# Performance work log

Measured on AMD Instinct MI355X. Metric: run time of the kernel, lower is better.

Reference implementation:

```python
import math
import jax, jax.numpy as jnp
import numpy as np

D_MODEL, N_HEADS, QKV, D_HEAD, D_FF, N_BLOCKS, IN_DIM = 288, 8, 328, 41, 1315, 4, 83
B, S = 1024, 128
EPS = 1e-5


def setup_inputs() -> dict:
    key = jax.random.key(0)
    ks = iter(jax.random.split(key, 64))
    def rn(shape, scale=0.05):
        return jax.random.normal(next(ks), shape, jnp.float32) * scale
    inp = {
        "x": jax.random.normal(next(ks), (B, S, IN_DIM), jnp.float32),
        "Wp": rn((D_MODEL, IN_DIM)), "bp": rn((D_MODEL,)),
        "phase": rn((D_MODEL,)),
        "Wq": rn((N_BLOCKS, QKV, D_MODEL)), "bq": rn((N_BLOCKS, QKV)),
        "Wk": rn((N_BLOCKS, QKV, D_MODEL)), "bk": rn((N_BLOCKS, QKV)),
        "Wv": rn((N_BLOCKS, QKV, D_MODEL)), "bv": rn((N_BLOCKS, QKV)),
        "Wo": rn((N_BLOCKS, D_MODEL, QKV)), "bo": rn((N_BLOCKS, D_MODEL)),
        "temp": jnp.ones((N_BLOCKS,), jnp.float32) + rn((N_BLOCKS,), 0.01),
        "qscale": jnp.ones((N_BLOCKS, N_HEADS), jnp.float32) + rn((N_BLOCKS, N_HEADS), 0.01),
        "Wf1": rn((N_BLOCKS, D_FF, D_MODEL)), "bf1": rn((N_BLOCKS, D_FF)),
        "Wf2": rn((N_BLOCKS, D_MODEL, D_FF)), "bf2": rn((N_BLOCKS, D_MODEL)),
        "n1w": jnp.ones((N_BLOCKS, D_MODEL), jnp.float32), "n1b": jnp.zeros((N_BLOCKS, D_MODEL), jnp.float32),
        "n2w": jnp.ones((N_BLOCKS, D_MODEL), jnp.float32), "n2b": jnp.zeros((N_BLOCKS, D_MODEL), jnp.float32),
        "skip": jnp.ones((N_BLOCKS,), jnp.float32),
        "bn_w": jnp.ones((D_MODEL,), jnp.float32), "bn_b": jnp.zeros((D_MODEL,), jnp.float32),
        "bn_mean": rn((D_MODEL,)), "bn_var": jax.random.uniform(next(ks), (D_MODEL,), jnp.float32, 0.5, 1.5),
        "h1w": rn((144, D_MODEL)), "h1b": rn((144,)),
        "h2w": rn((72, 144)), "h2b": rn((72,)),
        "h3w": rn((1, 72)), "h3b": rn((1,)),
        "u1w": rn((72, D_MODEL)), "u1b": rn((72,)),
        "u2w": rn((1, 72)), "u2b": rn((1,)),
    }
    return inp


def _layer_norm(x, w, b):
    mu = jnp.mean(x, axis=-1, keepdims=True)
    var = jnp.mean((x - mu) ** 2, axis=-1, keepdims=True)
    return (x - mu) * jax.lax.rsqrt(var + EPS) * w + b


def reference(x, Wp, bp, phase, Wq, bq, Wk, bk, Wv, bv, Wo, bo, temp, qscale,
              Wf1, bf1, Wf2, bf2, n1w, n1b, n2w, n2b, skip,
              bn_w, bn_b, bn_mean, bn_var,
              h1w, h1b, h2w, h2b, h3w, h3b, u1w, u1b, u2w, u2b):
    Bsz, Sl, _ = x.shape
    # input projection
    h = jnp.einsum('bsi,di->bsd', x, Wp) + bp
    # sinusoidal positional encoding modulated by cos(quantum_phase)
    pos = jnp.arange(Sl, dtype=jnp.float32)[:, None]
    div = jnp.exp(jnp.arange(0, D_MODEL, 2, dtype=jnp.float32) * (-math.log(10000.0) / D_MODEL))
    pe = jnp.zeros((Sl, D_MODEL), jnp.float32)
    pe = pe.at[:, 0::2].set(jnp.sin(pos * div)).at[:, 1::2].set(jnp.cos(pos * div))
    h = h + pe * jnp.cos(phase)

    for l in range(N_BLOCKS):
        # attention with temperature-scaled softmax + post-softmax per-head scale
        q = (jnp.einsum('bsd,qd->bsq', h, Wq[l]) + bq[l]).reshape(Bsz, Sl, N_HEADS, D_HEAD)
        k = (jnp.einsum('bsd,qd->bsq', h, Wk[l]) + bk[l]).reshape(Bsz, Sl, N_HEADS, D_HEAD)
        v = (jnp.einsum('bsd,qd->bsq', h, Wv[l]) + bv[l]).reshape(Bsz, Sl, N_HEADS, D_HEAD)
        scale = math.sqrt(D_HEAD) * temp[l]
        scores = jnp.einsum('bqhd,bkhd->bhqk', q, k) / scale  # [B,H,S,S]
        attn = jax.nn.softmax(scores, axis=-1) * qscale[l][None, :, None, None]
        o = jnp.einsum('bhqk,bkhd->bqhd', attn, v).reshape(Bsz, Sl, QKV)
        o = jnp.einsum('bsq,dq->bsd', o, Wo[l]) + bo[l]
        h = _layer_norm(h + skip[l] * o, n1w[l], n1b[l])
        # GELU FFN (exact erf gelu, dropout inactive in eval)
        f = jax.nn.gelu(jnp.einsum('bsd,fd->bsf', h, Wf1[l]) + bf1[l], approximate=False)
        f = jnp.einsum('bsf,df->bsd', f, Wf2[l]) + bf2[l]
        h = _layer_norm(h + f, n2w[l], n2b[l])

    pooled = jnp.mean(h, axis=1)  # [B, D_MODEL]
    # output head: BatchNorm1d (eval, running stats) -> GELU -> MLP
    z = (pooled - bn_mean) * jax.lax.rsqrt(bn_var + EPS) * bn_w + bn_b
    z = jax.nn.gelu(z, approximate=False)
    z = jax.nn.gelu(z @ h1w.T + h1b, approximate=False)
    z = jax.nn.gelu(z @ h2w.T + h2b, approximate=False)
    pred = z @ h3w.T + h3b  # [B, 1]
    # uncertainty head
    u = jax.nn.relu(pooled @ u1w.T + u1b)
    unc = jax.nn.softplus(u @ u2w.T + u2b)  # [B, 1]
    return pred, unc
```

## Files before the change

kernel.cpp:

```cpp
#include <hip/hip_runtime.h>
#include <cstdint>

typedef __attribute__((ext_vector_type(8))) short short8;
typedef __attribute__((ext_vector_type(4))) short s4v;
typedef __attribute__((ext_vector_type(4))) float floatx4;

#define DEV __device__ __forceinline__

DEV short f2bf(float f) {
  unsigned u = __builtin_bit_cast(unsigned, f);
  u += 0x7fffu + ((u >> 16) & 1u);
  return (short)(u >> 16);
}
DEV short f2bf_ru(float f) {
  unsigned u = __builtin_bit_cast(unsigned, f);
  return (short)((u + 0x8000u) >> 16);
}
DEV float bf2f(short s) {
  unsigned u = ((unsigned)(unsigned short)s) << 16;
  return __builtin_bit_cast(float, u);
}
DEV float gelu_exact(float x) {
  return 0.5f * x * (1.0f + erff(x * 0.70710678118654752f));
}
DEV float gelu_fast(float x) {
  const float t2 = 1.5957691216057308f * (x + 0.044715f * x * x * x);
  return x / (1.0f + __expf(-t2));
}
DEV void gload16(const void* g, void* l) {
  __builtin_amdgcn_global_load_lds((const __attribute__((address_space(1))) void*)g,
                                   (__attribute__((address_space(3))) void*)l,
                                   16, 0, 0);
}

DEV int stage_col64(int row, int g) {
  return ((g >> 2) ^ (row & 1)) * 32 + (((g & 3) ^ ((row >> 1) & 3))) * 8;
}
DEV int frag_off64(int R, int s, int quad) {
  return R * 64 + ((((s ^ (R & 1)) << 2) | (quad ^ ((R >> 1) & 3)))) * 8;
}

template<int MODE>
__global__ __launch_bounds__(256)
void gemm_kernel(const short* __restrict__ A, const short* __restrict__ Bw,
                 const float* __restrict__ bias, short* __restrict__ C,
                 const float* __restrict__ pe,
                 int K, int lda, int ldb, int ldc, int Nstore, int NT, long hstride)
{
  __shared__ __align__(16) short lds[128 * 136];
  short* Ct = lds;

  const int tid  = threadIdx.x;
  const int wave = tid >> 6, lane = tid & 63;
  const int quad = lane >> 4, r16 = lane & 15;
  const int per = gridDim.x >> 3;
  const int gti = (blockIdx.x & 7) * per + (blockIdx.x >> 3);
  const int mt = gti / NT, nt = gti - mt * NT;
  const int wm = (wave >> 1) * 64, wn = (wave & 1) * 64;

  const long Abase = (long)mt * 128 * lda;
  const long Bbase = (long)nt * 128 * ldb;

  floatx4 acc[4][4] = {};

  int k0 = 0;
  for (; k0 + 64 <= K; k0 += 64) {
    __syncthreads();
#pragma unroll
    for (int j = 0; j < 8; ++j) {
      const int c2 = tid + j * 256;
      const int cb = c2 & 1023;
      const int row = cb >> 3, g = cb & 7;
      const int col = stage_col64(row, g);
      const short* src = (c2 < 1024) ? (A  + Abase + (long)row * lda + k0 + col)
                                     : (Bw + Bbase + (long)row * ldb + k0 + col);
      gload16(src, &lds[(size_t)(c2 & ~63) * 8]);
    }
    __syncthreads();

#pragma unroll
    for (int s = 0; s < 2; ++s) {
      short8 af[4], bfr[4];
#pragma unroll
      for (int i = 0; i < 4; ++i) {
        const int R = wm + i * 16 + r16;
        af[i] = *(const short8*)&lds[frag_off64(R, s, quad)];
      }
#pragma unroll
      for (int j = 0; j < 4; ++j) {
        const int R = wn + j * 16 + r16;
        bfr[j] = *(const short8*)&lds[8192 + frag_off64(R, s, quad)];
      }
#pragma unroll
      for (int i = 0; i < 4; ++i)
#pragma unroll
        for (int j = 0; j < 4; ++j)
          acc[i][j] = __builtin_amdgcn_mfma_f32_16x16x32_bf16(bfr[j], af[i], acc[i][j], 0, 0, 0);
    }
  }

  if (k0 < K) {
    short* As = lds;
    short* Bs = lds + 128 * 32;
    const int row0 = tid >> 2,         cc0 = (tid & 3) ^ ((row0 >> 1) & 3);
    const int row1 = (256 + tid) >> 2, cc1 = ((256 + tid) & 3) ^ ((row1 >> 1) & 3);
    __syncthreads();
    gload16(A  + Abase + (long)row0 * lda + k0 + cc0 * 8, &As[(0 * 256 + wave * 64) * 8]);
    gload16(A  + Abase + (long)row1 * lda + k0 + cc1 * 8, &As[(1 * 256 + wave * 64) * 8]);
    gload16(Bw + Bbase + (long)row0 * ldb + k0 + cc0 * 8, &Bs[(0 * 256 + wave * 64) * 8]);
    gload16(Bw + Bbase + (long)row1 * ldb + k0 + cc1 * 8, &Bs[(1 * 256 + wave * 64) * 8]);
    __syncthreads();

    short8 af[4], bfr[4];
#pragma unroll
    for (int i = 0; i < 4; ++i) {
      const int R = wm + i * 16 + r16;
      af[i] = *(const short8*)&As[R * 32 + (quad ^ ((R >> 1) & 3)) * 8];
    }
#pragma unroll
    for (int j = 0; j < 4; ++j) {
      const int R = wn + j * 16 + r16;
      bfr[j] = *(const short8*)&Bs[R * 32 + (quad ^ ((R >> 1) & 3)) * 8];
    }
#pragma unroll
    for (int i = 0; i < 4; ++i)
#pragma unroll
      for (int j = 0; j < 4; ++j)
        acc[i][j] = __builtin_amdgcn_mfma_f32_16x16x32_bf16(bfr[j], af[i], acc[i][j], 0, 0, 0);
  }

  const int mb0 = mt * 128, tb = nt * 128;

  __syncthreads();
#pragma unroll
  for (int j = 0; j < 4; ++j) {
    const int n0 = wn + j * 16 + quad * 4;
    const floatx4 b4 = *(const floatx4*)&bias[tb + n0];
#pragma unroll
    for (int i = 0; i < 4; ++i) {
      const int m = wm + i * 16 + r16;
      floatx4 v = acc[i][j] + b4;
      if (MODE == 1) {
#pragma unroll
        for (int rg = 0; rg < 4; ++rg) v[rg] = gelu_fast(v[rg]);
      }
      if (MODE == 2) {
        const floatx4 p4 = *(const floatx4*)&pe[((mb0 + m) & 127) * 384 + tb + n0];
        v = v + p4;
      }
      s4v o4;
#pragma unroll
      for (int rg = 0; rg < 4; ++rg) o4[rg] = f2bf_ru(v[rg]);
      *(s4v*)&Ct[m * 136 + n0] = o4;
    }
  }
  __syncthreads();

#pragma unroll
  for (int rr = 0; rr < 8; ++rr) {
    const int chunk = rr * 256 + tid;
    const int row = chunk >> 4, ch = chunk & 15;
    const int gcol = tb + ch * 8;
    if (MODE == 3) {
      const int g = gcol / 48, d0 = gcol - g * 48;
      *(short8*)(C + (long)g * hstride + (long)(mb0 + row) * 48 + d0) =
          *(const short8*)&Ct[row * 136 + ch * 8];
    } else if (gcol < Nstore) {
      *(short8*)(C + (long)(mb0 + row) * ldc + gcol) = *(const short8*)&Ct[row * 136 + ch * 8];
    }
  }
}

template<bool AHEAD>
__global__ __launch_bounds__(512, 4)
void gemm_ln_kernel(const short* __restrict__ A, const short* __restrict__ Bw,
                    const float* __restrict__ bias, short* __restrict__ h,
                    const float* __restrict__ lnw, const float* __restrict__ lnb,
                    const float* __restrict__ skip_p, int layer, int use_skip,
                    int K, int lda, int ldb, long ahs)
{
  __shared__ __align__(16) short lds[128 * 296];
  __shared__ float redp[4][2][2][16];
  __shared__ float reds[4][2][2][16];
  short* Hs = lds;

  const int tid  = threadIdx.x;
  const int wave = tid >> 6, lane = tid & 63;
  const int quad = lane >> 4, r16 = lane & 15;
  const int wr = wave >> 1, wc = wave & 1;
  const int mt = blockIdx.x;
  const long mrow0 = (long)mt * 128;

  floatx4 acc[2][9] = {};

  auto stage = [&](short* buf, int k0) {
    for (int c = tid; c < 1664; c += 512) {
      const void* src;
      if (c < 512) {
        const int row = c >> 2, cc = (c & 3) ^ ((row >> 1) & 3);
        if (AHEAD) {
          const int kc = k0 + cc * 8;
          const int g = kc / 48, d = kc - g * 48;
          src = A + (long)g * ahs + (mrow0 + row) * 48 + d;
        } else {
          src = A + (mrow0 + row) * lda + k0 + cc * 8;
        }
      } else {
        const int cb = c - 512;
        const int row = cb >> 2, cc = (cb & 3) ^ ((row >> 1) & 3);
        src = Bw + (long)row * ldb + k0 + cc * 8;
      }
      gload16(src, &buf[(size_t)(c & ~63) * 8]);
    }
  };

  auto compute = [&](const short* buf) {
    const short* As_ = buf;
    const short* Bs_ = buf + 4096;
    const int Ra0 = wr * 32 + r16, Ra1 = Ra0 + 16;
    const short8 af0 = *(const short8*)&As_[Ra0 * 32 + (quad ^ ((Ra0 >> 1) & 3)) * 8];
    const short8 af1 = *(const short8*)&As_[Ra1 * 32 + (quad ^ ((Ra1 >> 1) & 3)) * 8];
#pragma unroll
    for (int t = 0; t < 9; ++t) {
      const int Rb = wc * 144 + t * 16 + r16;
      const short8 b = *(const short8*)&Bs_[Rb * 32 + (quad ^ ((Rb >> 1) & 3)) * 8];
      acc[0][t] = __builtin_amdgcn_mfma_f32_16x16x32_bf16(b, af0, acc[0][t], 0, 0, 0);
      acc[1][t] = __builtin_amdgcn_mfma_f32_16x16x32_bf16(b, af1, acc[1][t], 0, 0, 0);
    }
  };

  short* const B0 = lds;
  short* const B1 = lds + 13312;

  stage(B0, 0);
  __syncthreads();
  int k0 = 0;
  while (true) {
    if (k0 + 32 < K) stage(B1, k0 + 32);
    compute(B0);
    __syncthreads();
    k0 += 32;
    if (k0 >= K) break;
    if (k0 + 32 < K) stage(B0, k0 + 32);
    compute(B1);
    __syncthreads();
    k0 += 32;
    if (k0 >= K) break;
  }

  for (int c = tid; c < 4608; c += 512) {
    const int row = c / 36, ch = c - row * 36;
    *(short8*)&Hs[row * 296 + ch * 8] =
        *(const short8*)(h + (mrow0 + row) * 288 + ch * 8);
  }
  __syncthreads();

  const float skipv = use_skip ? skip_p[layer] : 1.0f;
  const int m0 = wr * 32 + r16, m1 = m0 + 16;

  float ps0 = 0.f, ss0 = 0.f, ps1 = 0.f, ss1 = 0.f;
#pragma unroll
  for (int t = 0; t < 9; ++t) {
    const int n0 = wc * 144 + t * 16 + quad * 4;
    const floatx4 b4 = *(const floatx4*)&bias[n0];
    const s4v h40 = *(const s4v*)&Hs[m0 * 296 + n0];
    const s4v h41 = *(const s4v*)&Hs[m1 * 296 + n0];
#pragma unroll
    for (int rg = 0; rg < 4; ++rg) {
      const float y0 = bf2f(h40[rg]) + skipv * (acc[0][t][rg] + b4[rg]);
      const float y1 = bf2f(h41[rg]) + skipv * (acc[1][t][rg] + b4[rg]);
      acc[0][t][rg] = y0; acc[1][t][rg] = y1;
      ps0 += y0; ss0 += y0 * y0;
      ps1 += y1; ss1 += y1 * y1;
    }
  }
  ps0 += __shfl_xor(ps0, 16); ps0 += __shfl_xor(ps0, 32);
  ss0 += __shfl_xor(ss0, 16); ss0 += __shfl_xor(ss0, 32);
  ps1 += __shfl_xor(ps1, 16); ps1 += __shfl_xor(ps1, 32);
  ss1 += __shfl_xor(ss1, 16); ss1 += __shfl_xor(ss1, 32);
  if (lane < 16) {
    redp[wr][wc][0][r16] = ps0; redp[wr][wc][1][r16] = ps1;
    reds[wr][wc][0][r16] = ss0; reds[wr][wc][1][r16] = ss1;
  }
  __syncthreads();
  const float psum0 = redp[wr][0][0][r16] + redp[wr][1][0][r16];
  const float psum1 = redp[wr][0][1][r16] + redp[wr][1][1][r16];
  const float ssum0 = reds[wr][0][0][r16] + reds[wr][1][0][r16];
  const float ssum1 = reds[wr][0][1][r16] + reds[wr][1][1][r16];
  const float mean0 = psum0 * (1.f / 288.f), mean1 = psum1 * (1.f / 288.f);
  const float rstd0 = rsqrtf(ssum0 * (1.f / 288.f) - mean0 * mean0 + 1e-5f);
  const float rstd1 = rsqrtf(ssum1 * (1.f / 288.f) - mean1 * mean1 + 1e-5f);

#pragma unroll
  for (int t = 0; t < 9; ++t) {
    const int n0 = wc * 144 + t * 16 + quad * 4;
    const floatx4 w4 = *(const floatx4*)&lnw[n0];
    const floatx4 l4 = *(const floatx4*)&lnb[n0];
    s4v o0, o1;
#pragma unroll
    for (int rg = 0; rg < 4; ++rg) {
      o0[rg] = f2bf_ru((acc[0][t][rg] - mean0) * rstd0 * w4[rg] + l4[rg]);
      o1[rg] = f2bf_ru((acc[1][t][rg] - mean1) * rstd1 * w4[rg] + l4[rg]);
    }
    *(s4v*)&Hs[m0 * 296 + n0] = o0;
    *(s4v*)&Hs[m1 * 296 + n0] = o1;
  }
  __syncthreads();

  for (int c = tid; c < 4608; c += 512) {
    const int row = c / 36, ch = c - row * 36;
    *(short8*)(h + (mrow0 + row) * 288 + ch * 8) =
        *(const short8*)&Hs[row * 296 + ch * 8];
  }
}

__global__ __launch_bounds__(512, 2)
void ffn_kernel(short* __restrict__ h,
                const short* __restrict__ W1, const float* __restrict__ b1,
                const short* __restrict__ W2, const float* __restrict__ b2,
                const float* __restrict__ lnw, const float* __restrict__ lnb)
{
  __shared__ __align__(16) short lds[53248];
  __shared__ float redp[4][2][2][16];
  __shared__ float reds[4][2][2][16];
  short* const fl = lds + 36864;

  const int tid  = threadIdx.x;
  const int wave = tid >> 6, lane = tid & 63;
  const int quad = lane >> 4, r16 = lane & 15;
  const int wr = wave >> 1, wp = wave & 1;
  const long mrow0 = (long)blockIdx.x * 128;

  short8 ha[2][9];
#pragma unroll
  for (int i = 0; i < 2; ++i) {
    const long rb = (mrow0 + wr * 32 + i * 16 + r16) * 288L;
#pragma unroll
    for (int k9 = 0; k9 < 9; ++k9)
      ha[i][k9] = *(const short8*)(h + rb + k9 * 32 + quad * 8);
  }

  floatx4 acc2[2][9] = {};

  auto stageW1_64 = [&](int c, int kp, short* dst) {
#pragma unroll
    for (int j = 0; j < 2; ++j) {
      const int c2 = tid + j * 512;
      const int row = c2 >> 3, g = c2 & 7;
      gload16(W1 + ((long)(c * 128 + row)) * 288 + kp * 64 + stage_col64(row, g),
              &dst[(size_t)(c2 & ~63) * 8]);
    }
  };
  auto stageW1_32 = [&](int c, int k9, short* dst) {
    const int row = tid >> 2, cc = (tid & 3) ^ ((row >> 1) & 3);
    gload16(W1 + ((long)(c * 128 + row)) * 288 + k9 * 32 + cc * 8,
            &dst[(size_t)(tid & ~63) * 8]);
  };
  auto stageW2_64 = [&](int c, int kh, short* dst) {
#pragma unroll
    for (int j = 0; j < 5; ++j) {
      const int c2 = tid + j * 512;
      if (c2 < 2304) {
        const int row = c2 >> 3, g = c2 & 7;
        gload16(W2 + (long)row * 1408 + c * 128 + kh * 64 + stage_col64(row, g),
                &dst[(size_t)(c2 & ~63) * 8]);
      }
    }
  };

  short* const ring0 = lds;
  short* const ring1 = lds + 18432;

  stageW1_64(0, 0, ring0);
  __syncthreads();
  int cur = 0;

  for (int c = 0; c < 11; ++c) {
    floatx4 acc1[2][4] = {};

#pragma unroll
    for (int kp = 0; kp < 4; ++kp) {
      short* const Sn = cur ? ring0 : ring1;
      const short* Sc = cur ? ring1 : ring0;
      if (kp < 3) stageW1_64(c, kp + 1, Sn);
      else        stageW1_32(c, 8, Sn);

#pragma unroll
      for (int s = 0; s < 2; ++s) {
        short8 bfr[4];
#pragma unroll
        for (int j = 0; j < 4; ++j) {
          const int R = wp * 64 + j * 16 + r16;
          bfr[j] = *(const short8*)&Sc[frag_off64(R, s, quad)];
        }
#pragma unroll
        for (int i = 0; i < 2; ++i)
#pragma unroll
          for (int j = 0; j < 4; ++j)
            acc1[i][j] = __builtin_amdgcn_mfma_f32_16x16x32_bf16(bfr[j], ha[i][kp * 2 + s], acc1[i][j], 0, 0, 0);
      }
      __syncthreads();
      cur ^= 1;
    }

    {
      short* const Sn = cur ? ring0 : ring1;
      const short* Sc = cur ? ring1 : ring0;
      stageW2_64(c, 0, Sn);

      short8 bfr[4];
#pragma unroll
      for (int j = 0; j < 4; ++j) {
        const int R = wp * 64 + j * 16 + r16;
        bfr[j] = *(const short8*)&Sc[R * 32 + (quad ^ ((R >> 1) & 3)) * 8];
      }
#pragma unroll
      for (int i = 0; i < 2; ++i)
#pragma unroll
        for (int j = 0; j < 4; ++j)
          acc1[i][j] = __builtin_amdgcn_mfma_f32_16x16x32_bf16(bfr[j], ha[i][8], acc1[i][j], 0, 0, 0);

#pragma unroll
      for (int i = 0; i < 2; ++i) {
        const int m = wr * 32 + i * 16 + r16;
#pragma unroll
        for (int j = 0; j < 4; ++j) {
          const int nb = c * 128 + wp * 64 + j * 16 + quad * 4;
          const floatx4 b4 = *(const floatx4*)&b1[nb];
          s4v o;
#pragma unroll
          for (int rg = 0; rg < 4; ++rg)
            o[rg] = f2bf_ru(gelu_fast(acc1[i][j][rg] + b4[rg]));
          const int ks = wp * 2 + (j >> 1);
          const int mg = ((j & 1) * 2 + (quad >> 1)) ^ ((m >> 1) & 3);
          *(s4v*)&fl[ks * 4096 + m * 32 + mg * 8 + (quad & 1) * 4] = o;
        }
      }
      __syncthreads();
      cur ^= 1;
    }

#pragma unroll
    for (int sg = 0; sg < 2; ++sg) {
      short* const Sn = cur ? ring0 : ring1;
      const short* Sc = cur ? ring1 : ring0;
      if (sg == 0)     stageW2_64(c, 1, Sn);
      else if (c < 10) stageW1_64(c + 1, 0, Sn);

#pragma unroll
      for (int s = 0; s < 2; ++s) {
        const int ks = sg * 2 + s;
        short8 af2[2];
#pragma unroll
        for (int i = 0; i < 2; ++i) {
          const int R = wr * 32 + i * 16 + r16;
          af2[i] = *(const short8*)&fl[ks * 4096 + R * 32 + (quad ^ ((R >> 1) & 3)) * 8];
        }
        short8 br[9];
#pragma unroll
        for (int t = 0; t < 9; ++t) {
          const int R = wp * 144 + t * 16 + r16;
          br[t] = *(const short8*)&Sc[frag_off64(R, s, quad)];
        }
#pragma unroll
        for (int i = 0; i < 2; ++i)
#pragma unroll
          for (int t = 0; t < 9; ++t)
            acc2[i][t] = __builtin_amdgcn_mfma_f32_16x16x32_bf16(br[t], af2[i], acc2[i][t], 0, 0, 0);
      }
      __syncthreads();
      cur ^= 1;
    }
  }

  for (int c2 = tid; c2 < 4608; c2 += 512) {
    const int row = c2 / 36, ch = c2 - row * 36;
    *(short8*)&lds[row * 296 + ch * 8] =
        *(const short8*)(h + (mrow0 + row) * 288 + ch * 8);
  }
  __syncthreads();

  const int m0 = wr * 32 + r16, m1 = m0 + 16;
  float ps0 = 0.f, ss0 = 0.f, ps1 = 0.f, ss1 = 0.f;
#pragma unroll
  for (int t = 0; t < 9; ++t) {
    const int n0 = wp * 144 + t * 16 + quad * 4;
    const floatx4 b4 = *(const floatx4*)&b2[n0];
    const s4v h40 = *(const s4v*)&lds[m0 * 296 + n0];
    const s4v h41 = *(const s4v*)&lds[m1 * 296 + n0];
#pragma unroll
    for (int rg = 0; rg < 4; ++rg) {
      const float y0 = bf2f(h40[rg]) + acc2[0][t][rg] + b4[rg];
      const float y1 = bf2f(h41[rg]) + acc2[1][t][rg] + b4[rg];
      acc2[0][t][rg] = y0; acc2[1][t][rg] = y1;
      ps0 += y0; ss0 += y0 * y0;
      ps1 += y1; ss1 += y1 * y1;
    }
  }
  ps0 += __shfl_xor(ps0, 16); ps0 += __shfl_xor(ps0, 32);
  ss0 += __shfl_xor(ss0, 16); ss0 += __shfl_xor(ss0, 32);
  ps1 += __shfl_xor(ps1, 16); ps1 += __shfl_xor(ps1, 32);
  ss1 += __shfl_xor(ss1, 16); ss1 += __shfl_xor(ss1, 32);
  if (lane < 16) {
    redp[wr][wp][0][r16] = ps0; redp[wr][wp][1][r16] = ps1;
    reds[wr][wp][0][r16] = ss0; reds[wr][wp][1][r16] = ss1;
  }
  __syncthreads();
  const float psum0 = redp[wr][0][0][r16] + redp[wr][1][0][r16];
  const float psum1 = redp[wr][0][1][r16] + redp[wr][1][1][r16];
  const float ssum0 = reds[wr][0][0][r16] + reds[wr][1][0][r16];
  const float ssum1 = reds[wr][0][1][r16] + reds[wr][1][1][r16];
  const float mean0 = psum0 * (1.f / 288.f), mean1 = psum1 * (1.f / 288.f);
  const float rstd0 = rsqrtf(ssum0 * (1.f / 288.f) - mean0 * mean0 + 1e-5f);
  const float rstd1 = rsqrtf(ssum1 * (1.f / 288.f) - mean1 * mean1 + 1e-5f);

#pragma unroll
  for (int t = 0; t < 9; ++t) {
    const int n0 = wp * 144 + t * 16 + quad * 4;
    const floatx4 w4 = *(const floatx4*)&lnw[n0];
    const floatx4 l4 = *(const floatx4*)&lnb[n0];
    s4v o0, o1;
#pragma unroll
    for (int rg = 0; rg < 4; ++rg) {
      o0[rg] = f2bf_ru((acc2[0][t][rg] - mean0) * rstd0 * w4[rg] + l4[rg]);
      o1[rg] = f2bf_ru((acc2[1][t][rg] - mean1) * rstd1 * w4[rg] + l4[rg]);
    }
    *(s4v*)&lds[m0 * 296 + n0] = o0;
    *(s4v*)&lds[m1 * 296 + n0] = o1;
  }
  __syncthreads();

  for (int c2 = tid; c2 < 4608; c2 += 512) {
    const int row = c2 / 36, ch = c2 - row * 36;
    *(short8*)(h + (mrow0 + row) * 288 + ch * 8) =
        *(const short8*)&lds[row * 296 + ch * 8];
  }
}

__global__ __launch_bounds__(256)
void attn_kernel(short* __restrict__ qkv,
                 const float* __restrict__ qscale, int layer, long Mc)
{
  __shared__ __align__(16) short qk[2 * 128 * 72];
  __shared__ __align__(16) short vsT[48 * 136 + 32];
  __shared__ float red[2][2][64];

  short* qs = qk;
  short* ks = qk + 128 * 72;
  short* Pb = qk;

  const int b = blockIdx.x, h = blockIdx.y;
  const int tid = threadIdx.x;
  const long sec = Mc * 48;
  const short* qg = qkv + (long)h * sec + (long)b * 128 * 48;
  const short* kg = qg + 8 * sec;
  const short* vg = qg + 16 * sec;
  short* og = qkv + (long)(16 + h) * sec + (long)b * 128 * 48;

  for (int c = tid; c < 768; c += 256) {
    const int s = c / 6, dc = c - (c / 6) * 6;
    *(short8*)&qs[s * 72 + dc * 8] = *(const short8*)(qg + (long)s * 48 + dc * 8);
    *(short8*)&ks[s * 72 + dc * 8] = *(const short8*)(kg + (long)s * 48 + dc * 8);
  }
  {
    short8 z;
#pragma unroll
    for (int j = 0; j < 8; ++j) z[j] = 0;
    for (int c = tid; c < 384; c += 256) {
      const int s = c / 3, t = c - (c / 3) * 3;
      *(short8*)&qs[s * 72 + 48 + t * 8] = z;
      *(short8*)&ks[s * 72 + 48 + t * 8] = z;
    }
  }
  for (int c = tid; c < 768; c += 256) {
    const int s = c & 127, dc = c >> 7;
    const short8 tv = *(const short8*)(vg + (long)s * 48 + dc * 8);
#pragma unroll
    for (int j = 0; j < 8; ++j) {
      const int row = dc * 8 + j;
      vsT[row * 136 + ((row >> 3) & 3) * 8 + s] = tv[j];
    }
  }
  __syncthreads();

  const int wave = tid >> 6, lane = tid & 63;
  const int quad = lane >> 4, r16 = lane & 15;
  const int wm = (wave >> 1) * 64, wn = (wave & 1) * 64;
  const int rh = wave >> 1, ch = wave & 1;
  const float qsc = qscale[layer * 8 + h];

  floatx4 acc[4][4] = {};
#pragma unroll
  for (int kk = 0; kk < 2; ++kk) {
    const int k0 = kk * 32;
    short8 af[4], bfr[4];
#pragma unroll
    for (int i = 0; i < 4; ++i)
      af[i] = *(const short8*)&qs[(wm + i * 16 + r16) * 72 + k0 + quad * 8];
#pragma unroll
    for (int j = 0; j < 4; ++j)
      bfr[j] = *(const short8*)&ks[(wn + j * 16 + r16) * 72 + k0 + quad * 8];
#pragma unroll
    for (int i = 0; i < 4; ++i)
#pragma unroll
      for (int j = 0; j < 4; ++j)
        acc[i][j] = __builtin_amdgcn_mfma_f32_16x16x32_bf16(bfr[j], af[i], acc[i][j], 0, 0, 0);
  }

  float rmax[4], rsum[4];
#pragma unroll
  for (int i = 0; i < 4; ++i) {
    float m = acc[i][0][0];
#pragma unroll
    for (int j = 0; j < 4; ++j)
#pragma unroll
      for (int rg = 0; rg < 4; ++rg) m = fmaxf(m, acc[i][j][rg]);
    m = fmaxf(m, __shfl_xor(m, 16));
    m = fmaxf(m, __shfl_xor(m, 32));
    rmax[i] = m;
  }
  if (lane < 16)
#pragma unroll
    for (int i = 0; i < 4; ++i) red[rh][ch][i * 16 + r16] = rmax[i];
  __syncthreads();
#pragma unroll
  for (int i = 0; i < 4; ++i)
    rmax[i] = fmaxf(red[rh][0][i * 16 + r16], red[rh][1][i * 16 + r16]);

#pragma unroll
  for (int i = 0; i < 4; ++i) {
    float s = 0.f;
#pragma unroll
    for (int j = 0; j < 4; ++j)
#pragma unroll
      for (int rg = 0; rg < 4; ++rg) {
        const float e = __expf(acc[i][j][rg] - rmax[i]);
        acc[i][j][rg] = e;
        s += e;
      }
    s += __shfl_xor(s, 16);
    s += __shfl_xor(s, 32);
    rsum[i] = s;
  }
  __syncthreads();
  if (lane < 16)
#pragma unroll
    for (int i = 0; i < 4; ++i) red[rh][ch][i * 16 + r16] = rsum[i];
  __syncthreads();
#pragma unroll
  for (int i = 0; i < 4; ++i)
    rmax[i] = qsc / (red[rh][0][i * 16 + r16] + red[rh][1][i * 16 + r16]);

#pragma unroll
  for (int i = 0; i < 4; ++i) {
    const int sq = wm + i * 16 + r16;
#pragma unroll
    for (int j = 0; j < 4; ++j) {
      const int sk0 = wn + j * 16 + quad * 4;
      s4v p4;
#pragma unroll
      for (int rg = 0; rg < 4; ++rg) p4[rg] = f2bf_ru(acc[i][j][rg] * rmax[i]);
      *(s4v*)&Pb[sq * 136 + sk0] = p4;
    }
  }
  __syncthreads();

  const int om = (wave >> 1) * 64, on = (wave & 1) * 32;
  const int jn = (on == 0) ? 2 : 1;
  floatx4 oacc[4][2] = {};
  for (int kk = 0; kk < 4; ++kk) {
    const int k0 = kk * 32;
    short8 af[4], bfr[2];
#pragma unroll
    for (int i = 0; i < 4; ++i)
      af[i] = *(const short8*)&Pb[(om + i * 16 + r16) * 136 + k0 + quad * 8];
    for (int j = 0; j < jn; ++j) {
      const int row = on + j * 16 + r16;
      bfr[j] = *(const short8*)&vsT[row * 136 + ((row >> 3) & 3) * 8 + k0 + quad * 8];
    }
#pragma unroll
    for (int i = 0; i < 4; ++i)
      for (int j = 0; j < jn; ++j)
        oacc[i][j] = __builtin_amdgcn_mfma_f32_16x16x32_bf16(bfr[j], af[i], oacc[i][j], 0, 0, 0);
  }
#pragma unroll
  for (int i = 0; i < 4; ++i)
    for (int j = 0; j < jn; ++j) {
      const int d0 = on + j * 16 + quad * 4;
      const int sq = om + i * 16 + r16;
      s4v o4;
#pragma unroll
      for (int rg = 0; rg < 4; ++rg) o4[rg] = f2bf_ru(oacc[i][j][rg]);
      *(s4v*)(og + (long)sq * 48 + d0) = o4;
    }
}

__global__ __launch_bounds__(256)
void head_kernel(const short* __restrict__ hb, float* __restrict__ out,
                 const float* bn_w, const float* bn_b, const float* bn_mean, const float* bn_var,
                 const float* h1w, const float* h1b, const float* h2w, const float* h2b,
                 const float* h3w, const float* h3b,
                 const float* u1w, const float* u1b, const float* u2w, const float* u2b)
{
  __shared__ float psum[252][8];
  __shared__ float pooled[288], z[288], z1[144], z2[72], uu[72];
  const int b = blockIdx.x, tid = threadIdx.x;

  if (tid < 252) {
    const int cch = tid % 36, grp = tid / 36;
    float a[8];
#pragma unroll
    for (int j = 0; j < 8; ++j) a[j] = 0.f;
    for (int r = grp; r < 128; r += 7) {
      const short8 hv = *(const short8*)(hb + ((long)b * 128 + r) * 288 + cch * 8);
#pragma unroll
      for (int j = 0; j < 8; ++j) a[j] += bf2f(hv[j]);
    }
#pragma unroll
    for (int j = 0; j < 8; ++j) psum[tid][j] = a[j];
  }
  __syncthreads();
  for (int d = tid; d < 288; d += 256) {
    const int cch = d >> 3, j = d & 7;
    float s = 0.f;
#pragma unroll
    for (int g = 0; g < 7; ++g) s += psum[g * 36 + cch][j];
    pooled[d] = s * (1.f / 128.f);
  }
  __syncthreads();

  for (int d = tid; d < 288; d += 256) {
    const float p = pooled[d];
    z[d] = gelu_exact((p - bn_mean[d]) * rsqrtf(bn_var[d] + 1e-5f) * bn_w[d] + bn_b[d]);
  }
  __syncthreads();

  if (tid < 144) {
    float s = h1b[tid];
    for (int k = 0; k < 288; ++k) s += z[k] * h1w[tid * 288 + k];
    z1[tid] = gelu_exact(s);
  } else if (tid < 216) {
    const int t = tid - 144;
    float s = u1b[t];
    for (int k = 0; k < 288; ++k) s += pooled[k] * u1w[t * 288 + k];
    uu[t] = fmaxf(s, 0.f);
  }
  __syncthreads();

  if (tid < 72) {
    float s = h2b[tid];
    for (int k = 0; k < 144; ++k) s += z1[k] * h2w[tid * 144 + k];
    z2[tid] = gelu_exact(s);
  }
  __syncthreads();

  if (tid == 0) {
    float s = h3b[0];
    for (int k = 0; k < 72; ++k) s += z2[k] * h3w[k];
    out[b] = s;
  }
  if (tid == 64) {
    float s = u2b[0];
    for (int k = 0; k < 72; ++k) s += uu[k] * u2w[k];
    out[1024 + b] = (s > 20.f) ? s : log1pf(__expf(s));
  }
}

__global__ void conv_w_kernel(const float* __restrict__ src, short* __restrict__ dst,
                              int N, int K, int Npad, int Kpad, int total)
{
  const int i = blockIdx.x * 256 + threadIdx.x;
  if (i >= total) return;
  const int kk = i % Kpad;
  const int t  = i / Kpad;
  const int n  = t % Npad;
  const int l  = t / Npad;
  const float v = (n < N && kk < K) ? src[((long)l * N + n) * K + kk] : 0.f;
  dst[i] = f2bf(v);
}

__global__ void conv_b_kernel(const float* __restrict__ src, float* __restrict__ dst,
                              int N, int Npad, int total)
{
  const int i = blockIdx.x * 256 + threadIdx.x;
  if (i >= total) return;
  const int n = i % Npad, l = i / Npad;
  dst[i] = (n < N) ? src[l * N + n] : 0.f;
}

__global__ void conv_wqkv_kernel(const float* __restrict__ Wq, const float* __restrict__ Wk,
                                 const float* __restrict__ Wv, const float* __restrict__ temp,
                                 short* __restrict__ dst)
{
  const int i = blockIdx.x * 256 + threadIdx.x;
  if (i >= 4 * 1152 * 288) return;
  const int kk = i % 288;
  const int t  = i / 288;
  const int r  = t % 1152;
  const int l  = t / 1152;
  const int g  = r / 48, d = r - (r / 48) * 48;
  const int sec = g >> 3, head = g & 7;
  float v = 0.f;
  if (d < 41) {
    const float* W = (sec == 0) ? Wq : (sec == 1) ? Wk : Wv;
    v = W[((long)l * 328 + head * 41 + d) * 288 + kk];
    if (sec == 0) v *= 1.0f / (6.4031242374328485f * temp[l]);
  }
  dst[i] = f2bf(v);
}

__global__ void conv_bqkv_kernel(const float* __restrict__ bq, const float* __restrict__ bk,
                                 const float* __restrict__ bv, const float* __restrict__ temp,
                                 float* __restrict__ dst)
{
  const int i = blockIdx.x * 256 + threadIdx.x;
  if (i >= 4 * 1152) return;
  const int r = i % 1152, l = i / 1152;
  const int g = r / 48, d = r - (r / 48) * 48;
  const int sec = g >> 3, head = g & 7;
  float v = 0.f;
  if (d < 41) {
    const float* b = (sec == 0) ? bq : (sec == 1) ? bk : bv;
    v = b[l * 328 + head * 41 + d];
    if (sec == 0) v *= 1.0f / (6.4031242374328485f * temp[l]);
  }
  dst[i] = v;
}

__global__ void conv_wo_kernel(const float* __restrict__ Wo, short* __restrict__ dst)
{
  const int i = blockIdx.x * 256 + threadIdx.x;
  if (i >= 4 * 288 * 384) return;
  const int kk = i % 384;
  const int t  = i / 384;
  const int n  = t % 288;
  const int l  = t / 288;
  const int head = kk / 48, d = kk - head * 48;
  float v = 0.f;
  if (d < 41) v = Wo[((long)l * 288 + n) * 328 + head * 41 + d];
  dst[i] = f2bf(v);
}

__global__ void conv_x_kernel(const float* __restrict__ x, short* __restrict__ xb, int total)
{
  const int i = blockIdx.x * 256 + threadIdx.x;
  if (i >= total) return;
  const int c = i % 96;
  const int r = i / 96;
  xb[i] = f2bf((c < 83) ? x[(long)r * 83 + c] : 0.f);
}

__global__ void pe_kernel(const float* __restrict__ phase, float* __restrict__ pe_mod)
{
  const int i = blockIdx.x * 256 + threadIdx.x;
  if (i >= 128 * 384) return;
  const int d = i % 384, s = i / 384;
  float out = 0.f;
  if (d < 288) {
    const int pair = d >> 1;
    const float divv = expf((float)(2 * pair) * (-9.210340371976184f / 288.f));
    const float arg = (float)s * divv;
    const float v = (d & 1) ? cosf(arg) : sinf(arg);
    out = v * cosf(phase[d]);
  }
  pe_mod[i] = out;
}

extern "C" void kernel_launch(void* const* d_in, const int* in_sizes, int n_in,
                              void* d_out, int out_size, void* d_ws, size_t ws_size,
                              hipStream_t stream)
{
  (void)in_sizes; (void)n_in; (void)out_size;

  const float* x     = (const float*)d_in[0];
  const float* Wp    = (const float*)d_in[1];
  const float* bp    = (const float*)d_in[2];
  const float* phase = (const float*)d_in[3];
  const float* Wq    = (const float*)d_in[4];
  const float* bq    = (const float*)d_in[5];
  const float* Wk    = (const float*)d_in[6];
  const float* bk    = (const float*)d_in[7];
  const float* Wv    = (const float*)d_in[8];
  const float* bv    = (const float*)d_in[9];
  const float* Wo    = (const float*)d_in[10];
  const float* bo    = (const float*)d_in[11];
  const float* temp  = (const float*)d_in[12];
  const float* qscale= (const float*)d_in[13];
  const float* Wf1   = (const float*)d_in[14];
  const float* bf1   = (const float*)d_in[15];
  const float* Wf2   = (const float*)d_in[16];
  const float* bf2   = (const float*)d_in[17];
  const float* n1w   = (const float*)d_in[18];
  const float* n1b   = (const float*)d_in[19];
  const float* n2w   = (const float*)d_in[20];
  const float* n2b   = (const float*)d_in[21];
  const float* skip  = (const float*)d_in[22];
  const float* bn_w  = (const float*)d_in[23];
  const float* bn_b  = (const float*)d_in[24];
  const float* bn_mean=(const float*)d_in[25];
  const float* bn_var= (const float*)d_in[26];
  const float* h1w   = (const float*)d_in[27];
  const float* h1b   = (const float*)d_in[28];
  const float* h2w   = (const float*)d_in[29];
  const float* h2b   = (const float*)d_in[30];
  const float* h3w   = (const float*)d_in[31];
  const float* h3b   = (const float*)d_in[32];
  const float* u1w   = (const float*)d_in[33];
  const float* u1b   = (const float*)d_in[34];
  const float* u2w   = (const float*)d_in[35];
  const float* u2b   = (const float*)d_in[36];

  char* ws = (char*)d_ws;
  size_t off = 0;
  auto alloc = [&](size_t n) -> char* {
    off = (off + 255) & ~(size_t)255;
    char* p = ws + off;
    off += n;
    return p;
  };

  const long M = 131072;

  short* h_bf   = (short*)alloc((size_t)M * 288 * 2);
  float* pe_mod = (float*)alloc(128 * 384 * 4);

  short* Wp_b   = (short*)alloc((size_t)384 * 96 * 2);
  short* Wqkv_b = (short*)alloc((size_t)4 * 1152 * 288 * 2);
  short* Wo_b   = (short*)alloc((size_t)4 * 288 * 384 * 2);
  short* Wf1_b  = (short*)alloc((size_t)4 * 1408 * 288 * 2);
  short* Wf2_b  = (short*)alloc((size_t)4 * 384 * 1408 * 2);

  float* bp_p   = (float*)alloc((size_t)384 * 4);
  float* bqkv_p = (float*)alloc((size_t)4 * 1152 * 4);
  float* bo_p   = (float*)alloc((size_t)4 * 384 * 4);
  float* bf1_p  = (float*)alloc((size_t)4 * 1408 * 4);
  float* bf2_p  = (float*)alloc((size_t)4 * 384 * 4);

  const size_t fixed = off;
  int NC = 1;
  while (NC < 16 && fixed + (size_t)(M / NC) * 2304 + (1u << 20) > ws_size) NC <<= 1;
  const long Mc = M / NC;
  const long sec = Mc * 48;

  char* R = alloc((size_t)Mc * 2304);
  short* qkv_bf = (short*)R;
  short* x_bfc  = (short*)R;

  const dim3 blk(256);

  auto conv_w = [&](const float* s, short* d, int N, int K, int Np, int Kp, int L) {
    const int total = L * Np * Kp;
    conv_w_kernel<<<dim3((total + 255) / 256), blk, 0, stream>>>(s, d, N, K, Np, Kp, total);
  };
  auto conv_b = [&](const float* s, float* d, int N, int Np, int L) {
    const int total = L * Np;
    conv_b_kernel<<<dim3((total + 255) / 256), blk, 0, stream>>>(s, d, N, Np, total);
  };
  conv_w(Wp,  Wp_b,  288,   83, 384,   96, 1);
  conv_wqkv_kernel<<<dim3((4 * 1152 * 288 + 255) / 256), blk, 0, stream>>>(Wq, Wk, Wv, temp, Wqkv_b);
  conv_wo_kernel<<<dim3((4 * 288 * 384 + 255) / 256), blk, 0, stream>>>(Wo, Wo_b);
  conv_w(Wf1, Wf1_b, 1315, 288, 1408, 288, 4);
  conv_w(Wf2, Wf2_b, 288, 1315, 384, 1408, 4);
  conv_b(bp,  bp_p,  288,  384, 1);
  conv_bqkv_kernel<<<dim3((4 * 1152 + 255) / 256), blk, 0, stream>>>(bq, bk, bv, temp, bqkv_p);
  conv_b(bo,  bo_p,  288,  384, 4);
  conv_b(bf1, bf1_p, 1315, 1408, 4);
  conv_b(bf2, bf2_p, 288,  384, 4);
  pe_kernel<<<dim3((128 * 384 + 255) / 256), blk, 0, stream>>>(phase, pe_mod);

  auto gemm = [&](int mode, const short* A, const short* Bmat, const float* bias,
                  short* C, const float* pe, int K, int lda, int ldb, int ldc,
                  int Nstore, int NT, long Mrows, long hstride) {
    const dim3 grid((unsigned)((Mrows / 128) * NT));
    switch (mode) {
      case 0: gemm_kernel<0><<<grid, blk, 0, stream>>>(A, Bmat, bias, C, pe, K, lda, ldb, ldc, Nstore, NT, hstride); break;
      case 1: gemm_kernel<1><<<grid, blk, 0, stream>>>(A, Bmat, bias, C, pe, K, lda, ldb, ldc, Nstore, NT, hstride); break;
      case 2: gemm_kernel<2><<<grid, blk, 0, stream>>>(A, Bmat, bias, C, pe, K, lda, ldb, ldc, Nstore, NT, hstride); break;
      default: gemm_kernel<3><<<grid, blk, 0, stream>>>(A, Bmat, bias, C, pe, K, lda, ldb, ldc, Nstore, NT, hstride); break;
    }
  };

  for (int c = 0; c < NC; ++c) {
    const float* x_c = x + (size_t)c * Mc * 83;
    short* h_c = h_bf + (size_t)c * Mc * 288;

    const int xtot = (int)(Mc * 96);
    conv_x_kernel<<<dim3((xtot + 255) / 256), blk, 0, stream>>>(x_c, x_bfc, xtot);

    gemm(2, x_bfc, Wp_b, bp_p, h_c, pe_mod, 96, 96, 96, 288, 288, 3, Mc, 0);

    for (int l = 0; l < 4; ++l) {
      const short* Wqkv_l = Wqkv_b + (size_t)l * 1152 * 288;
      const short* Wo_l   = Wo_b   + (size_t)l * 288 * 384;
      const short* Wf1_l  = Wf1_b  + (size_t)l * 1408 * 288;
      const short* Wf2_l  = Wf2_b  + (size_t)l * 384 * 1408;

      gemm(3, h_c, Wqkv_l, bqkv_p + l * 1152, qkv_bf, nullptr,
           288, 288, 288, 0, 1152, 9, Mc, sec);

      attn_kernel<<<dim3((unsigned)(Mc / 128), 8), blk, 0, stream>>>(
          qkv_bf, qscale, l, Mc);

      gemm_ln_kernel<true><<<dim3((unsigned)(Mc / 128)), dim3(512), 0, stream>>>(
          qkv_bf + 16 * sec, Wo_l, bo_p + l * 384, h_c, n1w + l * 288, n1b + l * 288,
          skip, l, 1, 384, 48, 384, sec);

      ffn_kernel<<<dim3((unsigned)(Mc / 128)), dim3(512), 0, stream>>>(
          h_c, Wf1_l, bf1_p + l * 1408, Wf2_l, bf2_p + l * 384,
          n2w + l * 288, n2b + l * 288);
    }
  }

  head_kernel<<<dim3(1024), blk, 0, stream>>>(h_bf, (float*)d_out,
      bn_w, bn_b, bn_mean, bn_var,
      h1w, h1b, h2w, h2b, h3w, h3b,
      u1w, u1b, u2w, u2b);
}
```

Measured before the change: 3.145 ms.

## Shrink FFN kernel LDS footprint to raise occupancy and restage tiles as K-halves

The FFN kernel's LDS ring buffers shrink. W2 is now staged in 32-wide K slices instead of 64-wide ones, and the LayerNorm epilogue works in two 64-row passes, which drops the LDS array from about 104KB to about 68KB. Launch bounds go from 2 to 4 blocks per CU. The 64-wide K tile layout is changed to two contiguous 32-wide halves in both the GEMM and the FFN kernels, replacing the XOR-interleaved stage_col64/frag_off64 scheme. In exchange there are more barriers per W2 chunk and a serialized epilogue, and the tighter launch bound may force register spilling, since each thread holds 18 accumulators plus 18 A fragments.

```diff
diff --git a/kernel.cpp b/kernel.cpp
--- a/kernel.cpp
+++ b/kernel.cpp
@@ -31,13 +31,6 @@
   __builtin_amdgcn_global_load_lds((const __attribute__((address_space(1))) void*)g,
                                    (__attribute__((address_space(3))) void*)l,
                                    16, 0, 0);
-}
-
-DEV int stage_col64(int row, int g) {
-  return ((g >> 2) ^ (row & 1)) * 32 + (((g & 3) ^ ((row >> 1) & 3))) * 8;
-}
-DEV int frag_off64(int R, int s, int quad) {
-  return R * 64 + ((((s ^ (R & 1)) << 2) | (quad ^ ((R >> 1) & 3)))) * 8;
 }
 
 template<int MODE>
@@ -69,12 +62,14 @@
 #pragma unroll
     for (int j = 0; j < 8; ++j) {
       const int c2 = tid + j * 256;
+      const int op = c2 >> 10;
       const int cb = c2 & 1023;
-      const int row = cb >> 3, g = cb & 7;
-      const int col = stage_col64(row, g);
-      const short* src = (c2 < 1024) ? (A  + Abase + (long)row * lda + k0 + col)
-                                     : (Bw + Bbase + (long)row * ldb + k0 + col);
-      gload16(src, &lds[(size_t)(c2 & ~63) * 8]);
+      const int half = cb >> 9;
+      const int sub = cb & 511;
+      const int row = sub >> 2, cc = (sub & 3) ^ ((row >> 1) & 3);
+      const short* src = op ? (Bw + Bbase + (long)row * ldb + k0 + half * 32 + cc * 8)
+                            : (A  + Abase + (long)row * lda + k0 + half * 32 + cc * 8);
+      gload16(src, &lds[(size_t)(op * 8192 + half * 4096 + (sub & ~63) * 8)]);
     }
     __syncthreads();
 
@@ -84,12 +79,12 @@
 #pragma unroll
       for (int i = 0; i < 4; ++i) {
         const int R = wm + i * 16 + r16;
-        af[i] = *(const short8*)&lds[frag_off64(R, s, quad)];
+        af[i] = *(const short8*)&lds[s * 4096 + R * 32 + (quad ^ ((R >> 1) & 3)) * 8];
       }
 #pragma unroll
       for (int j = 0; j < 4; ++j) {
         const int R = wn + j * 16 + r16;
-        bfr[j] = *(const short8*)&lds[8192 + frag_off64(R, s, quad)];
+        bfr[j] = *(const short8*)&lds[8192 + s * 4096 + R * 32 + (quad ^ ((R >> 1) & 3)) * 8];
       }
 #pragma unroll
       for (int i = 0; i < 4; ++i)
@@ -314,16 +309,16 @@
   }
 }
 
-__global__ __launch_bounds__(512, 2)
+__global__ __launch_bounds__(512, 4)
 void ffn_kernel(short* __restrict__ h,
                 const short* __restrict__ W1, const float* __restrict__ b1,
                 const short* __restrict__ W2, const float* __restrict__ b2,
                 const float* __restrict__ lnw, const float* __restrict__ lnb)
 {
-  __shared__ __align__(16) short lds[53248];
+  __shared__ __align__(16) short lds[34816];
   __shared__ float redp[4][2][2][16];
   __shared__ float reds[4][2][2][16];
-  short* const fl = lds + 36864;
+  short* const fl = lds + 18432;
 
   const int tid  = threadIdx.x;
   const int wave = tid >> 6, lane = tid & 63;
@@ -346,30 +341,27 @@
 #pragma unroll
     for (int j = 0; j < 2; ++j) {
       const int c2 = tid + j * 512;
-      const int row = c2 >> 3, g = c2 & 7;
-      gload16(W1 + ((long)(c * 128 + row)) * 288 + kp * 64 + stage_col64(row, g),
-              &dst[(size_t)(c2 & ~63) * 8]);
+      const int half = c2 >> 9, sub = c2 & 511;
+      const int row = sub >> 2, cc = (sub & 3) ^ ((row >> 1) & 3);
+      gload16(W1 + ((long)(c * 128 + row)) * 288 + kp * 64 + half * 32 + cc * 8,
+              &dst[(size_t)(half * 4096 + (sub & ~63) * 8)]);
     }
   };
-  auto stageW1_32 = [&](int c, int k9, short* dst) {
+  auto stageW1_32 = [&](int c, short* dst) {
     const int row = tid >> 2, cc = (tid & 3) ^ ((row >> 1) & 3);
-    gload16(W1 + ((long)(c * 128 + row)) * 288 + k9 * 32 + cc * 8,
+    gload16(W1 + ((long)(c * 128 + row)) * 288 + 256 + cc * 8,
             &dst[(size_t)(tid & ~63) * 8]);
   };
-  auto stageW2_64 = [&](int c, int kh, short* dst) {
-#pragma unroll
-    for (int j = 0; j < 5; ++j) {
-      const int c2 = tid + j * 512;
-      if (c2 < 2304) {
-        const int row = c2 >> 3, g = c2 & 7;
-        gload16(W2 + (long)row * 1408 + c * 128 + kh * 64 + stage_col64(row, g),
-                &dst[(size_t)(c2 & ~63) * 8]);
-      }
+  auto stageW2_32 = [&](int c, int ks, short* dst) {
+    for (int c2 = tid; c2 < 1152; c2 += 512) {
+      const int row = c2 >> 2, cc = (c2 & 3) ^ ((row >> 1) & 3);
+      gload16(W2 + (long)row * 1408 + c * 128 + ks * 32 + cc * 8,
+              &dst[(size_t)(c2 & ~63) * 8]);
     }
   };
 
   short* const ring0 = lds;
-  short* const ring1 = lds + 18432;
+  short* const ring1 = lds + 9216;
 
   stageW1_64(0, 0, ring0);
   __syncthreads();
@@ -383,7 +375,7 @@
       short* const Sn = cur ? ring0 : ring1;
       const short* Sc = cur ? ring1 : ring0;
       if (kp < 3) stageW1_64(c, kp + 1, Sn);
-      else        stageW1_32(c, 8, Sn);
+      else        stageW1_32(c, Sn);
 
 #pragma unroll
       for (int s = 0; s < 2; ++s) {
@@ -391,7 +383,7 @@
 #pragma unroll
         for (int j = 0; j < 4; ++j) {
           const int R = wp * 64 + j * 16 + r16;
-          bfr[j] = *(const short8*)&Sc[frag_off64(R, s, quad)];
+          bfr[j] = *(const short8*)&Sc[s * 4096 + R * 32 + (quad ^ ((R >> 1) & 3)) * 8];
         }
 #pragma unroll
         for (int i = 0; i < 2; ++i)
@@ -406,7 +398,7 @@
     {
       short* const Sn = cur ? ring0 : ring1;
       const short* Sc = cur ? ring1 : ring0;
-      stageW2_64(c, 0, Sn);
+      stageW2_32(c, 0, Sn);
 
       short8 bfr[4];
 #pragma unroll
@@ -441,99 +433,105 @@
     }
 
 #pragma unroll
-    for (int sg = 0; sg < 2; ++sg) {
+    for (int sg = 0; sg < 4; ++sg) {
       short* const Sn = cur ? ring0 : ring1;
       const short* Sc = cur ? ring1 : ring0;
-      if (sg == 0)     stageW2_64(c, 1, Sn);
+      if (sg < 3)      stageW2_32(c, sg + 1, Sn);
       else if (c < 10) stageW1_64(c + 1, 0, Sn);
 
-#pragma unroll
-      for (int s = 0; s < 2; ++s) {
-        const int ks = sg * 2 + s;
-        short8 af2[2];
-#pragma unroll
-        for (int i = 0; i < 2; ++i) {
-          const int R = wr * 32 + i * 16 + r16;
-          af2[i] = *(const short8*)&fl[ks * 4096 + R * 32 + (quad ^ ((R >> 1) & 3)) * 8];
-        }
-        short8 br[9];
-#pragma unroll
-        for (int t = 0; t < 9; ++t) {
-          const int R = wp * 144 + t * 16 + r16;
-          br[t] = *(const short8*)&Sc[frag_off64(R, s, quad)];
-        }
-#pragma unroll
-        for (int i = 0; i < 2; ++i)
-#pragma unroll
-          for (int t = 0; t < 9; ++t)
-            acc2[i][t] = __builtin_amdgcn_mfma_f32_16x16x32_bf16(br[t], af2[i], acc2[i][t], 0, 0, 0);
-      }
+      short8 af2[2];
+#pragma unroll
+      for (int i = 0; i < 2; ++i) {
+        const int R = wr * 32 + i * 16 + r16;
+        af2[i] = *(const short8*)&fl[sg * 4096 + R * 32 + (quad ^ ((R >> 1) & 3)) * 8];
+      }
+      short8 br[9];
+#pragma unroll
+      for (int t = 0; t < 9; ++t) {
+        const int R = wp * 144 + t * 16 + r16;
+        br[t] = *(const short8*)&Sc[R * 32 + (quad ^ ((R >> 1) & 3)) * 8];
+      }
+#pragma unroll
+      for (int i = 0; i < 2; ++i)
+#pragma unroll
+        for (int t = 0; t < 9; ++t)
+          acc2[i][t] = __builtin_amdgcn_mfma_f32_16x16x32_bf16(br[t], af2[i], acc2[i][t], 0, 0, 0);
+
       __syncthreads();
       cur ^= 1;
     }
   }
 
-  for (int c2 = tid; c2 < 4608; c2 += 512) {
-    const int row = c2 / 36, ch = c2 - row * 36;
-    *(short8*)&lds[row * 296 + ch * 8] =
-        *(const short8*)(h + (mrow0 + row) * 288 + ch * 8);
-  }
-  __syncthreads();
-
   const int m0 = wr * 32 + r16, m1 = m0 + 16;
-  float ps0 = 0.f, ss0 = 0.f, ps1 = 0.f, ss1 = 0.f;
-#pragma unroll
-  for (int t = 0; t < 9; ++t) {
-    const int n0 = wp * 144 + t * 16 + quad * 4;
-    const floatx4 b4 = *(const floatx4*)&b2[n0];
-    const s4v h40 = *(const s4v*)&lds[m0 * 296 + n0];
-    const s4v h41 = *(const s4v*)&lds[m1 * 296 + n0];
-#pragma unroll
-    for (int rg = 0; rg < 4; ++rg) {
-      const float y0 = bf2f(h40[rg]) + acc2[0][t][rg] + b4[rg];
-      const float y1 = bf2f(h41[rg]) + acc2[1][t][rg] + b4[rg];
-      acc2[0][t][rg] = y0; acc2[1][t][rg] = y1;
-      ps0 += y0; ss0 += y0 * y0;
-      ps1 += y1; ss1 += y1 * y1;
-    }
-  }
-  ps0 += __shfl_xor(ps0, 16); ps0 += __shfl_xor(ps0, 32);
-  ss0 += __shfl_xor(ss0, 16); ss0 += __shfl_xor(ss0, 32);
-  ps1 += __shfl_xor(ps1, 16); ps1 += __shfl_xor(ps1, 32);
-  ss1 += __shfl_xor(ss1, 16); ss1 += __shfl_xor(ss1, 32);
-  if (lane < 16) {
-    redp[wr][wp][0][r16] = ps0; redp[wr][wp][1][r16] = ps1;
-    reds[wr][wp][0][r16] = ss0; reds[wr][wp][1][r16] = ss1;
-  }
-  __syncthreads();
-  const float psum0 = redp[wr][0][0][r16] + redp[wr][1][0][r16];
-  const float psum1 = redp[wr][0][1][r16] + redp[wr][1][1][r16];
-  const float ssum0 = reds[wr][0][0][r16] + reds[wr][1][0][r16];
-  const float ssum1 = reds[wr][0][1][r16] + reds[wr][1][1][r16];
-  const float mean0 = psum0 * (1.f / 288.f), mean1 = psum1 * (1.f / 288.f);
-  const float rstd0 = rsqrtf(ssum0 * (1.f / 288.f) - mean0 * mean0 + 1e-5f);
-  const float rstd1 = rsqrtf(ssum1 * (1.f / 288.f) - mean1 * mean1 + 1e-5f);
-
-#pragma unroll
-  for (int t = 0; t < 9; ++t) {
-    const int n0 = wp * 144 + t * 16 + quad * 4;
-    const floatx4 w4 = *(const floatx4*)&lnw[n0];
-    const floatx4 l4 = *(const floatx4*)&lnb[n0];
-    s4v o0, o1;
-#pragma unroll
-    for (int rg = 0; rg < 4; ++rg) {
-      o0[rg] = f2bf_ru((acc2[0][t][rg] - mean0) * rstd0 * w4[rg] + l4[rg]);
-      o1[rg] = f2bf_ru((acc2[1][t][rg] - mean1) * rstd1 * w4[rg] + l4[rg]);
-    }
-    *(s4v*)&lds[m0 * 296 + n0] = o0;
-    *(s4v*)&lds[m1 * 296 + n0] = o1;
-  }
-  __syncthreads();
-
-  for (int c2 = tid; c2 < 4608; c2 += 512) {
-    const int row = c2 / 36, ch = c2 - row * 36;
-    *(short8*)(h + (mrow0 + row) * 288 + ch * 8) =
-        *(const short8*)&lds[row * 296 + ch * 8];
+#pragma unroll
+  for (int p = 0; p < 2; ++p) {
+    __syncthreads();
+    for (int c2 = tid; c2 < 2304; c2 += 512) {
+      const int row = c2 / 36, ch = c2 - row * 36;
+      *(short8*)&lds[row * 296 + ch * 8] =
+          *(const short8*)(h + (mrow0 + p * 64 + row) * 288 + ch * 8);
+    }
+    __syncthreads();
+
+    const bool act = (wr >> 1) == p;
+    if (act) {
+      const int lm0 = m0 - p * 64, lm1 = m1 - p * 64;
+      float ps0 = 0.f, ss0 = 0.f, ps1 = 0.f, ss1 = 0.f;
+#pragma unroll
+      for (int t = 0; t < 9; ++t) {
+        const int n0 = wp * 144 + t * 16 + quad * 4;
+        const floatx4 b4 = *(const floatx4*)&b2[n0];
+        const s4v h40 = *(const s4v*)&lds[lm0 * 296 + n0];
+        const s4v h41 = *(const s4v*)&lds[lm1 * 296 + n0];
+#pragma unroll
+        for (int rg = 0; rg < 4; ++rg) {
+          const float y0 = bf2f(h40[rg]) + acc2[0][t][rg] + b4[rg];
+          const float y1 = bf2f(h41[rg]) + acc2[1][t][rg] + b4[rg];
+          acc2[0][t][rg] = y0; acc2[1][t][rg] = y1;
+          ps0 += y0; ss0 += y0 * y0;
+          ps1 += y1; ss1 += y1 * y1;
+        }
+      }
+      ps0 += __shfl_xor(ps0, 16); ps0 += __shfl_xor(ps0, 32);
+      ss0 += __shfl_xor(ss0, 16); ss0 += __shfl_xor(ss0, 32);
+      ps1 += __shfl_xor(ps1, 16); ps1 += __shfl_xor(ps1, 32);
+      ss1 += __shfl_xor(ss1, 16); ss1 += __shfl_xor(ss1, 32);
+      if (lane < 16) {
+        redp[wr][wp][0][r16] = ps0; redp[wr][wp][1][r16] = ps1;
+        reds[wr][wp][0][r16] = ss0; reds[wr][wp][1][r16] = ss1;
+      }
+    }
+    __syncthreads();
+    if (act) {
+      const int lm0 = m0 - p * 64, lm1 = m1 - p * 64;
+      const float psum0 = redp[wr][0][0][r16] + redp[wr][1][0][r16];
+      const float psum1 = redp[wr][0][1][r16] + redp[wr][1][1][r16];
+      const float ssum0 = reds[wr][0][0][r16] + reds[wr][1][0][r16];
+      const float ssum1 = reds[wr][0][1][r16] + reds[wr][1][1][r16];
+      const float mean0 = psum0 * (1.f / 288.f), mean1 = psum1 * (1.f / 288.f);
+      const float rstd0 = rsqrtf(ssum0 * (1.f / 288.f) - mean0 * mean0 + 1e-5f);
+      const float rstd1 = rsqrtf(ssum1 * (1.f / 288.f) - mean1 * mean1 + 1e-5f);
+#pragma unroll
+      for (int t = 0; t < 9; ++t) {
+        const int n0 = wp * 144 + t * 16 + quad * 4;
+        const floatx4 w4 = *(const floatx4*)&lnw[n0];
+        const floatx4 l4 = *(const floatx4*)&lnb[n0];
+        s4v o0, o1;
+#pragma unroll
+        for (int rg = 0; rg < 4; ++rg) {
+          o0[rg] = f2bf_ru((acc2[0][t][rg] - mean0) * rstd0 * w4[rg] + l4[rg]);
+          o1[rg] = f2bf_ru((acc2[1][t][rg] - mean1) * rstd1 * w4[rg] + l4[rg]);
+        }
+        *(s4v*)&lds[lm0 * 296 + n0] = o0;
+        *(s4v*)&lds[lm1 * 296 + n0] = o1;
+      }
+    }
+    __syncthreads();
+    for (int c2 = tid; c2 < 2304; c2 += 512) {
+      const int row = c2 / 36, ch = c2 - row * 36;
+      *(short8*)(h + (mrow0 + p * 64 + row) * 288 + ch * 8) =
+          *(const short8*)&lds[row * 296 + ch * 8];
+    }
   }
 }
 
```

After: 5.293 ms. 1.68x slower.
